# Kernel tuning notes

Measured on AMD Instinct MI355X. Metric: run time of the kernel, lower is better.

## Reference

```python
import jax, jax.numpy as jnp
import numpy as np

N = 50000      # nodes
E = 500000     # edges
D_IN = 512
D_H = 512
D_OUT = 256


def setup_inputs() -> dict:
    key = jax.random.key(0)
    ks = jax.random.split(key, 5)
    x = jax.random.normal(ks[0], (N, D_IN), dtype=jnp.float32)
    edge_index = jax.random.randint(ks[1], (2, E), 0, N, dtype=jnp.int32)
    W1 = jax.random.normal(ks[2], (D_IN, D_H), dtype=jnp.float32) / np.float32(np.sqrt(D_IN))
    b1 = jnp.zeros((D_H,), dtype=jnp.float32)
    W2 = jax.random.normal(ks[3], (D_H, D_OUT), dtype=jnp.float32) / np.float32(np.sqrt(D_H))
    b2 = jnp.zeros((D_OUT,), dtype=jnp.float32)
    return {"x": x, "edge_index": edge_index, "W1": W1, "b1": b1, "W2": W2, "b2": b2}


def _gcn_conv(x, src, dst, W, b, n):
    # PyG GCNConv: h = X W; add self-loops; symmetric norm D^-1/2 (A+I) D^-1/2; aggregate at dst; + bias
    h = x @ W
    loop = jnp.arange(n, dtype=src.dtype)
    src_sl = jnp.concatenate([src, loop])
    dst_sl = jnp.concatenate([dst, loop])
    deg = jax.ops.segment_sum(jnp.ones_like(src_sl, dtype=h.dtype), dst_sl, num_segments=n)
    dinv = jnp.where(deg > 0, jax.lax.rsqrt(deg), 0.0)
    norm = dinv[src_sl] * dinv[dst_sl]                     # [E+N]
    msg = h[src_sl] * norm[:, None]                        # [E+N, out]
    out = jax.ops.segment_sum(msg, dst_sl, num_segments=n) # [N, out]
    return out + b


def reference(x, edge_index, W1, b1, W2, b2):
    # Encoder.forward in eval mode (dropout = identity, bn='none' = identity), ELU activation after each conv.
    src, dst = edge_index[0], edge_index[1]
    h = _gcn_conv(x, src, dst, W1, b1, N)
    h = jax.nn.elu(h)
    h = _gcn_conv(h, src, dst, W2, b2, N)
    return jax.nn.elu(h)
```

## Files before the change

### kernel.cpp

```cpp
#include <hip/hip_runtime.h>
#include <math.h>

#define N_NODES 50000
#define N_EDGES 500000
#define D_IN 512
#define D_H  512
#define D_OUT 256
#define NB 196
#define NBK 1954

typedef __attribute__((ext_vector_type(8))) short bf16x8;
typedef __attribute__((ext_vector_type(8))) unsigned short ushort8;
typedef __attribute__((ext_vector_type(4))) float f32x4;

__device__ __forceinline__ float b2f(unsigned short u) {
    union { unsigned int i; float f; } v; v.i = ((unsigned int)u) << 16; return v.f;
}
__device__ __forceinline__ unsigned short f2b(float f) {
    unsigned int x = __float_as_uint(f);
    unsigned int r = (x + 0x7fffu + ((x >> 16) & 1u)) >> 16;
    return (unsigned short)r;
}


__global__ __launch_bounds__(256) void k_zero(int* __restrict__ p, int n) {
    int i = blockIdx.x * 256 + threadIdx.x;
    if (i < n) p[i] = 0;
}


#define W1B  256
#define W2B  128

__global__ __launch_bounds__(256) void k_prep(const float* __restrict__ W1,
                                              unsigned short* __restrict__ W1t,
                                              const float* __restrict__ W2,
                                              unsigned short* __restrict__ W2t,
                                              const int* __restrict__ dst,
                                              int* __restrict__ indeg) {
    __shared__ float t[32][33];
    int b = blockIdx.x;
    const int tid = threadIdx.x;

    if (b < NBK) {
        const int e = b * 256 + tid;
        if (e < N_EDGES) atomicAdd(&indeg[dst[e]], 1);
        return;
    }
    b -= NBK;
    const float* W;
    unsigned short* Wt;
    int K, N, idx;
    if (b < W1B) { W = W1; Wt = W1t; K = D_IN; N = D_H; idx = b; }
    else         { W = W2; Wt = W2t; K = D_H; N = D_OUT; idx = b - W1B; }
    const int nkb = K / 32;
    const int bk = (idx % nkb) * 32;
    const int bn = (idx / nkb) * 32;
    const int tx = tid & 31, ty = tid >> 5;
    for (int i = ty; i < 32; i += 8) t[i][tx] = W[(size_t)(bk + i) * N + bn + tx];
    __syncthreads();
    for (int i = ty; i < 32; i += 8)
        Wt[(size_t)(bn + i) * K + bk + tx] = f2b(t[tx][i]);
}


__global__ __launch_bounds__(256) void k_partials(const int* __restrict__ indeg,
                                                  int* __restrict__ bsum) {
    __shared__ int wsum[4];
    const int tid = threadIdx.x, lane = tid & 63, w = tid >> 6;
    const int i = blockIdx.x * 256 + tid;
    int v = (i < N_NODES) ? indeg[i] : 0;
#pragma unroll
    for (int o = 32; o > 0; o >>= 1) v += __shfl_down(v, o, 64);
    if (lane == 0) wsum[w] = v;
    __syncthreads();
    if (tid == 0) bsum[blockIdx.x] = wsum[0] + wsum[1] + wsum[2] + wsum[3];
}

__global__ __launch_bounds__(256) void k_scanb(const int* __restrict__ bsum,
                                               int* __restrict__ boff) {
    __shared__ int wsum[4];
    const int tid = threadIdx.x, lane = tid & 63, w = tid >> 6;
    const int v = (tid < NB) ? bsum[tid] : 0;
    int s = v;
#pragma unroll
    for (int o = 1; o < 64; o <<= 1) {
        int t = __shfl_up(s, o, 64);
        if (lane >= o) s += t;
    }
    if (lane == 63) wsum[w] = s;
    __syncthreads();
    int add = 0;
    for (int k = 0; k < w; ++k) add += wsum[k];
    if (tid < NB) boff[tid] = add + s - v;
}

__global__ __launch_bounds__(256) void k_finalize(const int* __restrict__ indeg,
                                                  const int* __restrict__ boff,
                                                  int* __restrict__ row_start,
                                                  int* __restrict__ cursor,
                                                  float* __restrict__ dinv) {
    __shared__ int wsum[4];
    const int tid = threadIdx.x, lane = tid & 63, w = tid >> 6;
    const int i = blockIdx.x * 256 + tid;
    const int v = (i < N_NODES) ? indeg[i] : 0;
    int s = v;
#pragma unroll
    for (int o = 1; o < 64; o <<= 1) {
        int t = __shfl_up(s, o, 64);
        if (lane >= o) s += t;
    }
    if (lane == 63) wsum[w] = s;
    __syncthreads();
    int add = boff[blockIdx.x];
    for (int k = 0; k < w; ++k) add += wsum[k];
    if (i < N_NODES) {
        const int excl = add + s - v;
        row_start[i] = excl;
        cursor[i] = excl;
        dinv[i] = rsqrtf((float)(1 + v));
    }
    if (i == N_NODES) row_start[N_NODES] = N_EDGES;
}


__device__ __forceinline__ void gload16(const void* g, void* l) {
    __builtin_amdgcn_global_load_lds(
        (const __attribute__((address_space(1))) unsigned int*)g,
        (__attribute__((address_space(3))) unsigned int*)l, 16, 0, 0);
}

template <bool A32, bool FUSE_BUCKET>
__global__ __launch_bounds__(256, 4) void k_gemm(const void* __restrict__ Av,
                                                 const unsigned short* __restrict__ Bt,
                                                 unsigned short* __restrict__ C,
                                                 const float* __restrict__ rowscale,
                                                 int M, int N, int K,
                                                 int ncb, int nrb,
                                                 const int* __restrict__ src,
                                                 const int* __restrict__ dst,
                                                 int* __restrict__ cursor,
                                                 int* __restrict__ csr_src) {
    __shared__ __align__(16) short lds[16384];

    if (FUSE_BUCKET && blockIdx.x < NBK) {
        const int e = blockIdx.x * 256 + threadIdx.x;
        if (e < N_EDGES) {
            const int pos = atomicAdd(&cursor[dst[e]], 1);
            csr_src[pos] = src[e];
        }
        return;
    }
    const int bid = blockIdx.x - (FUSE_BUCKET ? NBK : 0);
    const int xcd = bid & 7;
    const int sidx = bid >> 3;
    const int cb = sidx % ncb;
    const int rb = (sidx / ncb) * 8 + xcd;
    if (rb >= nrb) return;
    const int brow = rb * 128;
    const int bcol = cb * 128;

    const int tid = threadIdx.x;
    const int wid = tid >> 6;
    const int lane = tid & 63;
    const int wr = wid >> 1, wc = wid & 1;
    const int lhi = lane >> 4, llo = lane & 15;

    const float* Af = (const float*)Av;
    const unsigned short* Ab = (const unsigned short*)Av;

    f32x4 acc[4][4];
#pragma unroll
    for (int i = 0; i < 4; ++i)
#pragma unroll
        for (int j = 0; j < 4; ++j) acc[i][j] = (f32x4){0.f, 0.f, 0.f, 0.f};

    float4 ar[2][2];

#define STAGE_A16(buf, kt)                                                      \
    {                                                                           \
        _Pragma("unroll") for (int g = 0; g < 2; ++g) {                         \
            const int s = g * 256 + tid;                                        \
            const int row = s >> 2;                                             \
            const int sc = (s & 3) ^ ((s >> 3) & 3);                            \
            int gr = brow + row; gr = gr < M ? gr : M - 1;                      \
            gload16(Ab + (size_t)gr * K + (kt) + sc * 8,                        \
                    &lds[(buf) * 4096 + (g * 256 + wid * 64) * 8]);             \
        }                                                                       \
    }
#define STAGE_B(buf, kt)                                                        \
    {                                                                           \
        _Pragma("unroll") for (int g = 0; g < 2; ++g) {                         \
            const int s = g * 256 + tid;                                        \
            const int row = s >> 2;                                             \
            const int sc = (s & 3) ^ ((s >> 3) & 3);                            \
            gload16(Bt + (size_t)(bcol + row) * K + (kt) + sc * 8,              \
                    &lds[8192 + (buf) * 4096 + (g * 256 + wid * 64) * 8]);      \
        }                                                                       \
    }
#define LOAD_A32(kt)                                                            \
    {                                                                           \
        _Pragma("unroll") for (int g = 0; g < 2; ++g) {                         \
            const int s = g * 256 + tid;                                        \
            const int row = s >> 2;                                             \
            const int sc = (s & 3) ^ ((s >> 3) & 3);                            \
            int gr = brow + row; gr = gr < M ? gr : M - 1;                      \
            const float* p = Af + (size_t)gr * K + (kt) + sc * 8;               \
            ar[g][0] = *(const float4*)p;                                       \
            ar[g][1] = *(const float4*)(p + 4);                                 \
        }                                                                       \
    }
#define WRITE_A32(buf)                                                          \
    {                                                                           \
        _Pragma("unroll") for (int g = 0; g < 2; ++g) {                         \
            ushort8 u;                                                          \
            u[0] = f2b(ar[g][0].x); u[1] = f2b(ar[g][0].y);                     \
            u[2] = f2b(ar[g][0].z); u[3] = f2b(ar[g][0].w);                     \
            u[4] = f2b(ar[g][1].x); u[5] = f2b(ar[g][1].y);                     \
            u[6] = f2b(ar[g][1].z); u[7] = f2b(ar[g][1].w);                     \
            *(ushort8*)&lds[(buf) * 4096 + (g * 256 + tid) * 8] = u;            \
        }                                                                       \
    }

    const int nt = K / 32;

    if (A32) {
        LOAD_A32(0);
        STAGE_B(0, 0);
        WRITE_A32(0);
    } else {
        STAGE_A16(0, 0);
        STAGE_B(0, 0);
    }
    __syncthreads();

    int cur = 0;
    for (int t = 0; t < nt; ++t) {
        const bool more = (t + 1 < nt);
        if (more) {
            if (A32) {
                LOAD_A32((t + 1) * 32);
            } else {
                STAGE_A16(cur ^ 1, (t + 1) * 32);
            }
            STAGE_B(cur ^ 1, (t + 1) * 32);
        }

        bf16x8 af[4], bf[4];
#pragma unroll
        for (int mi = 0; mi < 4; ++mi) {
            const int row = wr * 64 + mi * 16 + llo;
            af[mi] = *(const bf16x8*)&lds[cur * 4096 + row * 32 + ((lhi ^ ((row >> 1) & 3)) * 8)];
        }
#pragma unroll
        for (int ni = 0; ni < 4; ++ni) {
            const int row = wc * 64 + ni * 16 + llo;
            bf[ni] = *(const bf16x8*)&lds[8192 + cur * 4096 + row * 32 + ((lhi ^ ((row >> 1) & 3)) * 8)];
        }
#pragma unroll
        for (int mi = 0; mi < 4; ++mi)
#pragma unroll
            for (int ni = 0; ni < 4; ++ni)
                acc[mi][ni] = __builtin_amdgcn_mfma_f32_16x16x32_bf16(
                    af[mi], bf[ni], acc[mi][ni], 0, 0, 0);

        if (A32 && more) WRITE_A32(cur ^ 1);

        __syncthreads();
        cur ^= 1;
    }
#undef STAGE_A16
#undef STAGE_B
#undef LOAD_A32
#undef WRITE_A32

    short* cws = &lds[wid * 4096];

#pragma unroll
    for (int mi = 0; mi < 4; ++mi) {
#pragma unroll
        for (int r = 0; r < 4; ++r) {
            const int lrow = mi * 16 + lhi * 4 + r;
            int grow = brow + wr * 64 + lrow;
            grow = grow < M ? grow : M - 1;
            const float ds = rowscale[grow];
#pragma unroll
            for (int ni = 0; ni < 4; ++ni) {
                const int col = ni * 16 + llo;
                const int chunk = (col >> 3) ^ (lrow & 7);
                cws[lrow * 64 + chunk * 8 + (col & 7)] = (short)f2b(acc[mi][ni][r] * ds);
            }
        }
    }
    __syncthreads();

    {
        const int rsub = lane >> 3;
        const int c = lane & 7;
#pragma unroll
        for (int i = 0; i < 8; ++i) {
            const int row = i * 8 + rsub;
            const ushort8 o = *(const ushort8*)&cws[row * 64 + ((c ^ (row & 7)) * 8)];
            const int grow = brow + wr * 64 + row;
            if (grow < M)
                *(ushort8*)(C + (size_t)grow * N + bcol + wc * 64 + c * 8) = o;
        }
    }
}


template <int D, bool BF16_OUT>
__global__ __launch_bounds__(256) void k_aggregate(const unsigned short* __restrict__ H,
                                                   const float* __restrict__ bias,
                                                   void* __restrict__ outv,
                                                   const int* __restrict__ row_start,
                                                   const int* __restrict__ csr_src,
                                                   const float* __restrict__ dinv) {
    const int wid = threadIdx.x >> 6;
    const int lane = threadIdx.x & 63;
    int n, c0;
    if (D == 512) { n = blockIdx.x * 4 + wid; c0 = lane * 8; }
    else          { n = blockIdx.x * 8 + wid * 2 + (lane >> 5); c0 = (lane & 31) * 8; }
    if (n >= N_NODES) return;

    float acc[8];
    {
        ushort8 v = *(const ushort8*)(H + (size_t)n * D + c0);
#pragma unroll
        for (int e = 0; e < 8; ++e) acc[e] = b2f(v[e]);
    }

    const int e0 = row_start[n];
    const int e1 = row_start[n + 1];
    int j = e0;
    for (; j + 8 <= e1; j += 8) {
        int s[8];
#pragma unroll
        for (int q = 0; q < 8; ++q) s[q] = csr_src[j + q];
#pragma unroll
        for (int h = 0; h < 2; ++h) {
            const ushort8 v0 = *(const ushort8*)(H + (size_t)s[h * 4 + 0] * D + c0);
            const ushort8 v1 = *(const ushort8*)(H + (size_t)s[h * 4 + 1] * D + c0);
            const ushort8 v2 = *(const ushort8*)(H + (size_t)s[h * 4 + 2] * D + c0);
            const ushort8 v3 = *(const ushort8*)(H + (size_t)s[h * 4 + 3] * D + c0);
#pragma unroll
            for (int e = 0; e < 8; ++e) {
                acc[e] += b2f(v0[e]);
                acc[e] += b2f(v1[e]);
                acc[e] += b2f(v2[e]);
                acc[e] += b2f(v3[e]);
            }
        }
    }
    for (; j + 4 <= e1; j += 4) {
        const int s0 = csr_src[j + 0];
        const int s1 = csr_src[j + 1];
        const int s2 = csr_src[j + 2];
        const int s3 = csr_src[j + 3];
        const ushort8 v0 = *(const ushort8*)(H + (size_t)s0 * D + c0);
        const ushort8 v1 = *(const ushort8*)(H + (size_t)s1 * D + c0);
        const ushort8 v2 = *(const ushort8*)(H + (size_t)s2 * D + c0);
        const ushort8 v3 = *(const ushort8*)(H + (size_t)s3 * D + c0);
#pragma unroll
        for (int e = 0; e < 8; ++e) {
            acc[e] += b2f(v0[e]);
            acc[e] += b2f(v1[e]);
            acc[e] += b2f(v2[e]);
            acc[e] += b2f(v3[e]);
        }
    }
    for (; j < e1; ++j) {
        const int s = csr_src[j];
        const ushort8 v = *(const ushort8*)(H + (size_t)s * D + c0);
#pragma unroll
        for (int e = 0; e < 8; ++e) acc[e] += b2f(v[e]);
    }

    const float di = dinv[n];
#pragma unroll
    for (int e = 0; e < 8; ++e) {
        float t = fmaf(acc[e], di, bias[c0 + e]);
        acc[e] = t > 0.f ? t : expf(t) - 1.f;
    }

    if (BF16_OUT) {
        ushort8 o;
#pragma unroll
        for (int e = 0; e < 8; ++e) o[e] = f2b(acc[e]);
        *(ushort8*)((unsigned short*)outv + (size_t)n * D + c0) = o;
    } else {
        float* orow = (float*)outv + (size_t)n * D + c0;
        *(float4*)orow = make_float4(acc[0], acc[1], acc[2], acc[3]);
        *(float4*)(orow + 4) = make_float4(acc[4], acc[5], acc[6], acc[7]);
    }
}


extern "C" void kernel_launch(void* const* d_in, const int* in_sizes, int n_in,
                              void* d_out, int out_size, void* d_ws, size_t ws_size,
                              hipStream_t stream) {
    const float* x  = (const float*)d_in[0];
    const int* ei   = (const int*)d_in[1];
    const int* src  = ei;
    const int* dst  = ei + N_EDGES;
    const float* W1 = (const float*)d_in[2];
    const float* b1 = (const float*)d_in[3];
    const float* W2 = (const float*)d_in[4];
    const float* b2 = (const float*)d_in[5];
    float* out = (float*)d_out;

    char* ws = (char*)d_ws;
    size_t off = 0;
    auto alloc = [&](size_t bytes) -> void* {
        void* p = ws + off;
        off = (off + bytes + 255) & ~(size_t)255;
        return p;
    };
    int*   indeg     = (int*)alloc((size_t)N_NODES * 4);
    int*   bsum      = (int*)alloc((size_t)NB * 4);
    int*   boff      = (int*)alloc((size_t)NB * 4);
    int*   row_start = (int*)alloc((size_t)(N_NODES + 1) * 4);
    int*   cursor    = (int*)alloc((size_t)N_NODES * 4);
    int*   csr_src   = (int*)alloc((size_t)N_EDGES * 4);
    float* dinv      = (float*)alloc((size_t)N_NODES * 4);
    unsigned short* W1t  = (unsigned short*)alloc((size_t)D_H * D_IN * 2);
    unsigned short* W2t  = (unsigned short*)alloc((size_t)D_OUT * D_H * 2);
    unsigned short* H1   = (unsigned short*)alloc((size_t)N_NODES * D_H * 2);
    unsigned short* out1 = (unsigned short*)alloc((size_t)N_NODES * D_H * 2);
    unsigned short* H2   = (unsigned short*)alloc((size_t)N_NODES * D_OUT * 2);

    k_zero<<<NB, 256, 0, stream>>>(indeg, N_NODES);
    k_prep<<<NBK + W1B + W2B, 256, 0, stream>>>(W1, W1t, W2, W2t, dst, indeg);
    k_partials<<<NB, 256, 0, stream>>>(indeg, bsum);
    k_scanb<<<1, 256, 0, stream>>>(bsum, boff);
    k_finalize<<<NB, 256, 0, stream>>>(indeg, boff, row_start, cursor, dinv);

    const int nrb = (N_NODES + 127) / 128;
    const int rgrp = (nrb + 7) / 8;

    {
        const int ncb = D_H / 128;
        k_gemm<true, true><<<NBK + 8 * ncb * rgrp, 256, 0, stream>>>(
            x, W1t, H1, dinv, N_NODES, D_H, D_IN, ncb, nrb, src, dst, cursor, csr_src);
    }
    k_aggregate<512, true><<<(N_NODES + 3) / 4, 256, 0, stream>>>(H1, b1, out1, row_start, csr_src, dinv);

    {
        const int ncb = D_OUT / 128;
        k_gemm<false, false><<<8 * ncb * rgrp, 256, 0, stream>>>(
            out1, W2t, H2, dinv, N_NODES, D_OUT, D_H, ncb, nrb, nullptr, nullptr, nullptr, nullptr);
    }
    k_aggregate<256, false><<<(N_NODES + 7) / 8, 256, 0, stream>>>(H2, b2, out, row_start, csr_src, dinv);
}
```

Before: 268.9 us.

## Triple-buffer GEMM K-loop with explicit waitcnt and replace zero kernel with memset

The GEMM main loop moves from double buffering to a three-stage prefetch: loads for tile t+2 are issued while tile t is computed, and manual s_waitcnt vmcnt counts plus raw s_barrier replace __syncthreads. This is meant to hide more global-load latency behind the MFMA work. For the bf16 A path, A and B each get a third LDS buffer and occupancy is lowered to 3 blocks. The fp32 A path keeps register staging with a two-buffer A ring. The custom zero kernel is also replaced by hipMemsetAsync, which adds some risk that the hand-tuned wait counts are wrong or that the larger LDS footprint costs occupancy.

New measurement: 273.9 us. Within noise of the previous version (+1.9%).

```diff
diff --git a/kernel.cpp b/kernel.cpp
--- a/kernel.cpp
+++ b/kernel.cpp
@@ -20,12 +20,6 @@
     unsigned int x = __float_as_uint(f);
     unsigned int r = (x + 0x7fffu + ((x >> 16) & 1u)) >> 16;
     return (unsigned short)r;
-}
-
-
-__global__ __launch_bounds__(256) void k_zero(int* __restrict__ p, int n) {
-    int i = blockIdx.x * 256 + threadIdx.x;
-    if (i < n) p[i] = 0;
 }
 
 
@@ -131,17 +125,20 @@
 }
 
 template <bool A32, bool FUSE_BUCKET>
-__global__ __launch_bounds__(256, 4) void k_gemm(const void* __restrict__ Av,
-                                                 const unsigned short* __restrict__ Bt,
-                                                 unsigned short* __restrict__ C,
-                                                 const float* __restrict__ rowscale,
-                                                 int M, int N, int K,
-                                                 int ncb, int nrb,
-                                                 const int* __restrict__ src,
-                                                 const int* __restrict__ dst,
-                                                 int* __restrict__ cursor,
-                                                 int* __restrict__ csr_src) {
-    __shared__ __align__(16) short lds[16384];
+__global__ __launch_bounds__(256, A32 ? 4 : 3)
+void k_gemm(const void* __restrict__ Av,
+            const unsigned short* __restrict__ Bt,
+            unsigned short* __restrict__ C,
+            const float* __restrict__ rowscale,
+            int M, int N, int K,
+            int ncb, int nrb,
+            const int* __restrict__ src,
+            const int* __restrict__ dst,
+            int* __restrict__ cursor,
+            int* __restrict__ csr_src) {
+    constexpr int ABUFS = A32 ? 2 : 3;
+    constexpr int BBASE = ABUFS * 4096;
+    __shared__ __align__(16) short lds[(ABUFS + 3) * 4096];
 
     if (FUSE_BUCKET && blockIdx.x < NBK) {
         const int e = blockIdx.x * 256 + threadIdx.x;
@@ -177,7 +174,7 @@
 
     float4 ar[2][2];
 
-#define STAGE_A16(buf, kt)                                                      \
+#define STAGE_A16(bufidx, kt)                                                   \
     {                                                                           \
         _Pragma("unroll") for (int g = 0; g < 2; ++g) {                         \
             const int s = g * 256 + tid;                                        \
@@ -185,17 +182,17 @@
             const int sc = (s & 3) ^ ((s >> 3) & 3);                            \
             int gr = brow + row; gr = gr < M ? gr : M - 1;                      \
             gload16(Ab + (size_t)gr * K + (kt) + sc * 8,                        \
-                    &lds[(buf) * 4096 + (g * 256 + wid * 64) * 8]);             \
+                    &lds[(bufidx) * 4096 + (g * 256 + wid * 64) * 8]);          \
         }                                                                       \
     }
-#define STAGE_B(buf, kt)                                                        \
+#define STAGE_B(bufidx, kt)                                                     \
     {                                                                           \
         _Pragma("unroll") for (int g = 0; g < 2; ++g) {                         \
             const int s = g * 256 + tid;                                        \
             const int row = s >> 2;                                             \
             const int sc = (s & 3) ^ ((s >> 3) & 3);                            \
             gload16(Bt + (size_t)(bcol + row) * K + (kt) + sc * 8,              \
-                    &lds[8192 + (buf) * 4096 + (g * 256 + wid * 64) * 8]);      \
+                    &lds[BBASE + (bufidx) * 4096 + (g * 256 + wid * 64) * 8]);  \
         }                                                                       \
     }
 #define LOAD_A32(kt)                                                            \
@@ -210,7 +207,7 @@
             ar[g][1] = *(const float4*)(p + 4);                                 \
         }                                                                       \
     }
-#define WRITE_A32(buf)                                                          \
+#define WRITE_A32(bufidx)                                                       \
     {                                                                           \
         _Pragma("unroll") for (int g = 0; g < 2; ++g) {                         \
             ushort8 u;                                                          \
@@ -218,7 +215,7 @@
             u[2] = f2b(ar[g][0].z); u[3] = f2b(ar[g][0].w);                     \
             u[4] = f2b(ar[g][1].x); u[5] = f2b(ar[g][1].y);                     \
             u[6] = f2b(ar[g][1].z); u[7] = f2b(ar[g][1].w);                     \
-            *(ushort8*)&lds[(buf) * 4096 + (g * 256 + tid) * 8] = u;            \
+            *(ushort8*)&lds[(bufidx) * 4096 + (g * 256 + tid) * 8] = u;         \
         }                                                                       \
     }
 
@@ -228,34 +225,45 @@
         LOAD_A32(0);
         STAGE_B(0, 0);
         WRITE_A32(0);
+        LOAD_A32(32);
+        STAGE_B(1, 32);
+        asm volatile("s_waitcnt vmcnt(6) lgkmcnt(0)" ::: "memory");
     } else {
         STAGE_A16(0, 0);
         STAGE_B(0, 0);
-    }
-    __syncthreads();
-
-    int cur = 0;
+        STAGE_A16(1, 32);
+        STAGE_B(1, 32);
+        asm volatile("s_waitcnt vmcnt(4) lgkmcnt(0)" ::: "memory");
+    }
+    __builtin_amdgcn_s_barrier();
+    __builtin_amdgcn_sched_barrier(0);
+
+    int b0 = 0, b1 = 1, b2 = 2;
     for (int t = 0; t < nt; ++t) {
-        const bool more = (t + 1 < nt);
-        if (more) {
-            if (A32) {
-                LOAD_A32((t + 1) * 32);
-            } else {
-                STAGE_A16(cur ^ 1, (t + 1) * 32);
+        if (A32) {
+            if (t + 1 < nt) WRITE_A32((t + 1) & 1);
+            if (t + 2 < nt) {
+                LOAD_A32((t + 2) * 32);
+                STAGE_B(b2, (t + 2) * 32);
             }
-            STAGE_B(cur ^ 1, (t + 1) * 32);
+        } else {
+            if (t + 2 < nt) {
+                STAGE_A16(b2, (t + 2) * 32);
+                STAGE_B(b2, (t + 2) * 32);
+            }
         }
 
         bf16x8 af[4], bf[4];
+        const int abase = A32 ? ((t & 1) * 4096) : (b0 * 4096);
 #pragma unroll
         for (int mi = 0; mi < 4; ++mi) {
             const int row = wr * 64 + mi * 16 + llo;
-            af[mi] = *(const bf16x8*)&lds[cur * 4096 + row * 32 + ((lhi ^ ((row >> 1) & 3)) * 8)];
+            af[mi] = *(const bf16x8*)&lds[abase + row * 32 + ((lhi ^ ((row >> 1) & 3)) * 8)];
         }
 #pragma unroll
         for (int ni = 0; ni < 4; ++ni) {
             const int row = wc * 64 + ni * 16 + llo;
-            bf[ni] = *(const bf16x8*)&lds[8192 + cur * 4096 + row * 32 + ((lhi ^ ((row >> 1) & 3)) * 8)];
+            bf[ni] = *(const bf16x8*)&lds[BBASE + b0 * 4096 + row * 32 + ((lhi ^ ((row >> 1) & 3)) * 8)];
         }
 #pragma unroll
         for (int mi = 0; mi < 4; ++mi)
@@ -264,10 +272,16 @@
                 acc[mi][ni] = __builtin_amdgcn_mfma_f32_16x16x32_bf16(
                     af[mi], bf[ni], acc[mi][ni], 0, 0, 0);
 
-        if (A32 && more) WRITE_A32(cur ^ 1);
-
-        __syncthreads();
-        cur ^= 1;
+        if (t + 2 < nt) {
+            if (A32) asm volatile("s_waitcnt vmcnt(6) lgkmcnt(0)" ::: "memory");
+            else     asm volatile("s_waitcnt vmcnt(4) lgkmcnt(0)" ::: "memory");
+        } else {
+            asm volatile("s_waitcnt vmcnt(0) lgkmcnt(0)" ::: "memory");
+        }
+        __builtin_amdgcn_s_barrier();
+        __builtin_amdgcn_sched_barrier(0);
+
+        const int tmp = b0; b0 = b1; b1 = b2; b2 = tmp;
     }
 #undef STAGE_A16
 #undef STAGE_B
@@ -429,7 +443,7 @@
     unsigned short* out1 = (unsigned short*)alloc((size_t)N_NODES * D_H * 2);
     unsigned short* H2   = (unsigned short*)alloc((size_t)N_NODES * D_OUT * 2);
 
-    k_zero<<<NB, 256, 0, stream>>>(indeg, N_NODES);
+    hipMemsetAsync(indeg, 0, (size_t)N_NODES * 4, stream);
     k_prep<<<NBK + W1B + W2B, 256, 0, stream>>>(W1, W1t, W2, W2t, dst, indeg);
     k_partials<<<NB, 256, 0, stream>>>(indeg, bsum);
     k_scanb<<<1, 256, 0, stream>>>(bsum, boff);
```
